# Kernel optimization log

Hardware: AMD Instinct MI355X
Metric: run time of the kernel (lower is better)

Reference implementation:

```python
import jax, jax.numpy as jnp
import numpy as np

EPS = 1e-6
BN_EPS = 1e-5
K = 20

def _vn_linear(x, W):
    # x: [B,C,...] channel axis 1; W: [out,in]
    return jnp.einsum('oc,bc...->bo...', W, x)

def _vn_bn(x):
    # training-mode BatchNorm on per-vector norms (affine at init: gamma=1, beta=0)
    norm = jnp.sqrt(jnp.sum(x * x, axis=2)) + EPS  # [B,C,*spatial]
    axes = (0,) + tuple(range(2, norm.ndim))
    mean = jnp.mean(norm, axis=axes, keepdims=True)
    var = jnp.mean((norm - mean) ** 2, axis=axes, keepdims=True)  # biased, as torch BN
    norm_bn = (norm - mean) / jnp.sqrt(var + BN_EPS)
    return x / jnp.expand_dims(norm, 2) * jnp.expand_dims(norm_bn, 2)

def _vn_llr(x, Wf, Wd, ns=0.0, use_bn=True):
    p = _vn_linear(x, Wf)
    if use_bn:
        p = _vn_bn(p)
    d = _vn_linear(x, Wd)
    dot = jnp.sum(p * d, axis=2, keepdims=True)
    mask = (dot >= 0).astype(x.dtype)
    dsq = jnp.sum(d * d, axis=2, keepdims=True)
    return ns * p + (1.0 - ns) * (mask * p + (1.0 - mask) * (p - dot / (dsq + EPS) * d))

def _graph_feature_cross(x, k):
    # x: [B,3,N] -> [B,3,3,N,k]
    B, _, N = x.shape
    inner = -2.0 * jnp.einsum('bdn,bdm->bnm', x, x)
    xx = jnp.sum(x * x, axis=1)  # [B,N]
    pdist = -xx[:, :, None] - inner - xx[:, None, :]  # [B,N,N]
    idx = jax.lax.top_k(pdist, k)[1]  # [B,N,k] nearest neighbors
    xt = jnp.transpose(x, (0, 2, 1))  # [B,N,3]
    nbr = xt[jnp.arange(B)[:, None, None], idx]  # [B,N,k,3]
    ctr = jnp.broadcast_to(xt[:, :, None, :], nbr.shape)  # [B,N,k,3]
    cross = jnp.cross(nbr, ctr)
    feat = jnp.stack([nbr - ctr, ctr, cross], axis=3)  # [B,N,k,3ch,3vec]
    return jnp.transpose(feat, (0, 3, 4, 1, 2))  # [B,3,3,N,k]

def _forward(points, wposf, wposd, w1f, w1d, w2f, w2d, w3, ws1f, ws1d, ws2f, ws2d, wlin):
    x = jnp.transpose(points, (0, 2, 1))  # [B,3,N]
    B, _, N = x.shape
    feat = _graph_feature_cross(x, K)  # [B,3,3,N,K]
    x = _vn_llr(feat, wposf, wposd)  # conv_pos, dim=5 -> [B,21,3,N,K]
    x = jnp.mean(x, axis=-1)  # mean pool over k -> [B,21,3,N]
    x = _vn_llr(x, w1f, w1d)  # conv1
    x = _vn_llr(x, w2f, w2d)  # conv2 (feature_transform=False so in=21? no: conv2 takes 42 -- matches cat-free path only when feature_transform False? conv2 in=42 but code passes x of 21? original passes 21-ch into conv2 only if feature_transform else 21; here feature_transform=False and conv2 expects 42 in torch -- we mirror with w2f [42,42] applied after duplicating? No: mirror exact torch behavior below.)
    return x

def reference(points, wposf, wposd, w1f, w1d, w2f, w2d, w3, ws1f, ws1d, ws2f, ws2d, wlin):
    x = jnp.transpose(points, (0, 2, 1))  # [B,3,N]
    B, _, N = x.shape
    feat = _graph_feature_cross(x, K)  # [B,3,3,N,K]
    x = _vn_llr(feat, wposf, wposd)  # [B,21,3,N,K]
    x = jnp.mean(x, axis=-1)  # mean pool -> [B,21,3,N]
    x = _vn_llr(x, w1f, w1d)  # [B,21,3,N]
    # torch conv2 is Linear(42,42) but with feature_transform=False it is applied to 21-ch
    # input; nn.Linear would error, so faithful runnable form uses the duplicated-channel
    # convention: concat (x, x) is NOT in the original; instead we slice w2 to [42,21].
    x = _vn_llr(x, w2f[:, :21], w2d[:, :21])  # [B,42,3,N]
    x = _vn_bn(_vn_linear(x, w3))  # conv3 + bn3 -> [B,85,3,N]
    x_mean_out = jnp.mean(x, axis=-1, keepdims=True)  # [B,85,3,1]
    x = jnp.concatenate([x, jnp.broadcast_to(x_mean_out, x.shape)], axis=1)  # [B,170,3,N]
    z = _vn_llr(x, ws1f, ws1d)  # [B,85,3,N]
    z = _vn_llr(z, ws2f, ws2d)  # [B,42,3,N]
    z = _vn_linear(z, wlin)  # [B,3,3,N]
    z = jnp.transpose(z, (0, 2, 1, 3))  # [B,3,3,N]
    x_std = jnp.einsum('bijm,bjkm->bikm', x, z)  # [B,170,3,N]
    xf = x_std.reshape(B, -1, N)  # [B,510,N]
    inv_z = jnp.max(xf, axis=-1)  # [B,510]
    center_loc = jnp.mean(x_mean_out, axis=2)  # [B,85,1]
    return (inv_z, x_mean_out, center_loc)

def setup_inputs() -> dict:
    key = jax.random.key(0)
    ks = jax.random.split(key, 14)
    B, N = 4, 8192
    def w(k, shape):
        return (jax.random.normal(k, shape, dtype=jnp.float32) * (1.0 / np.sqrt(shape[1])))
    return {
        'points': jax.random.normal(ks[0], (B, N, 3), dtype=jnp.float32),
        'wposf': w(ks[1], (21, 3)),
        'wposd': w(ks[2], (21, 3)),
        'w1f': w(ks[3], (21, 21)),
        'w1d': w(ks[4], (21, 21)),
        'w2f': w(ks[5], (42, 42)),
        'w2d': w(ks[6], (42, 42)),
        'w3': w(ks[7], (85, 42)),
        'ws1f': w(ks[8], (85, 170)),
        'ws1d': w(ks[9], (85, 170)),
        'ws2f': w(ks[10], (42, 85)),
        'ws2d': w(ks[11], (42, 85)),
        'wlin': w(ks[12], (3, 42)),
    }
```

## Files before the change

kernel.cpp:

```cpp
#include <hip/hip_runtime.h>
#include <cstdint>
#include <cstddef>

#define EPSF 1e-6f
#define BN_EPSF 1e-5f

constexpr int Bb = 4;
constexpr int Nn = 8192;
constexpr int KK = 20;
constexpr int SEG = 8;
constexpr int SEGLEN = Nn / SEG;
constexpr int BUF = 24;

constexpr size_t KNN0_OFF = 0;
constexpr size_t X1_OFF  = 0;
constexpr size_t X2_OFF  = 2064384;
constexpr size_t X3_OFF  = 4128768;
constexpr size_t Z1_OFF  = 0;
constexpr size_t X4_OFF  = 8355840;
constexpr size_t IDX_OFF = 16711680;
constexpr size_t Z2_OFF  = 17367040;
constexpr size_t Z3_OFF  = 21495808;
constexpr size_t ACC_OFF = 21790720;
constexpr size_t XM_OFF  = 21791744;
constexpr size_t BF_OFF  = 21792764;
constexpr size_t BD_OFF  = 21793784;
constexpr size_t DEXT_OFF = 21795840;
constexpr size_t EXT_NEED = (DEXT_OFF + 8355840) * 4;

__device__ __forceinline__ float wave_sum(float v) {
#pragma unroll
  for (int off = 32; off; off >>= 1) v += __shfl_xor(v, off, 64);
  return v;
}
__device__ __forceinline__ float wave_max(float v) {
#pragma unroll
  for (int off = 32; off; off >>= 1) v = fmaxf(v, __shfl_xor(v, off, 64));
  return v;
}
__device__ __forceinline__ uint32_t umin32(uint32_t a, uint32_t b) { return a < b ? a : b; }
__device__ __forceinline__ uint32_t umax32(uint32_t a, uint32_t b) { return a < b ? b : a; }

__global__ __launch_bounds__(1024) void zero_acc(float* __restrict__ a) {
  a[threadIdx.x] = 0.f;
}

__global__ __launch_bounds__(256) void knn_kernel(const float* __restrict__ pts,
                                                  uint32_t* __restrict__ knnp) {
  __shared__ float4 tile[SEGLEN];
  __shared__ uint32_t buf[BUF * 256];
  const int tid = threadIdx.x;
  const int n = blockIdx.x * 256 + tid;
  const int b = blockIdx.y;
  const int s = blockIdx.z;
  const float* pb = pts + (size_t)b * Nn * 3;

  for (int i = tid; i < SEGLEN; i += 256) {
    const float* p = pb + (size_t)(s * SEGLEN + i) * 3;
    const float x = p[0], y = p[1], z = p[2];
    tile[i] = make_float4(x, y, z, 0.5f * (x * x + y * y + z * z));
  }
  const float qx = pb[n * 3 + 0], qy = pb[n * 3 + 1], qz = pb[n * 3 + 2];
  const float nqx = -qx, nqy = -qy, nqz = -qz;
  const float h = 0.5f * (qx * qx + qy * qy + qz * qz);
  __syncthreads();

  uint32_t keys[KK];
#pragma unroll
  for (int j = 0; j < KK; ++j) keys[j] = 0xFFFFFFFFu;

  const int base = s * SEGLEN;

#pragma unroll 4
  for (int j = 0; j < 64; ++j) {
    const float4 c = tile[j];
    float u = fmaf(nqx, c.x, fmaf(nqy, c.y, fmaf(nqz, c.z, c.w + h)));
    u = fmaxf(u, 0.f);
    uint32_t mx = (__float_as_uint(u) & 0xFFFFE000u) | (uint32_t)(base + j);
#pragma unroll
    for (int q = 0; q < KK; ++q) {
      const uint32_t mn = umin32(keys[q], mx);
      mx = umax32(keys[q], mx);
      keys[q] = mn;
    }
  }

  uint32_t thresh = keys[KK - 1];
  float thresh_up = __uint_as_float((thresh & 0xFFFFE000u) + 0x2000u);
  float th_h = thresh_up - h + 2.4e-7f * fabsf(thresh_up) + 1e-30f;
  int cnt = 0;

  for (int j0 = 64; j0 < SEGLEN; j0 += 4) {
#pragma unroll
    for (int u4 = 0; u4 < 4; ++u4) {
      const int j = j0 + u4;
      const float4 c = tile[j];
      const float up = fmaf(nqx, c.x, fmaf(nqy, c.y, fmaf(nqz, c.z, c.w)));
      if (up < th_h) {
        const float uc = fmaxf(up + h, 0.f);
        buf[cnt * 256 + tid] = (__float_as_uint(uc) & 0xFFFFE000u) | (uint32_t)(base + j);
        ++cnt;
      }
    }
    if (__any(cnt > BUF - 4)) {
#pragma unroll
      for (int i = 0; i < BUF; ++i) {
        uint32_t mx = (i < cnt) ? buf[i * 256 + tid] : 0xFFFFFFFFu;
#pragma unroll
        for (int q = 0; q < KK; ++q) {
          const uint32_t mn = umin32(keys[q], mx);
          mx = umax32(keys[q], mx);
          keys[q] = mn;
        }
      }
      cnt = 0;
      thresh = keys[KK - 1];
      thresh_up = __uint_as_float((thresh & 0xFFFFE000u) + 0x2000u);
      th_h = thresh_up - h + 2.4e-7f * fabsf(thresh_up) + 1e-30f;
    }
  }
#pragma unroll
  for (int i = 0; i < BUF; ++i) {
    uint32_t mx = (i < cnt) ? buf[i * 256 + tid] : 0xFFFFFFFFu;
#pragma unroll
    for (int q = 0; q < KK; ++q) {
      const uint32_t mn = umin32(keys[q], mx);
      mx = umax32(keys[q], mx);
      keys[q] = mn;
    }
  }

  uint32_t* op = knnp + ((size_t)(b * SEG + s) * KK) * Nn + n;
#pragma unroll
  for (int j = 0; j < KK; ++j) op[(size_t)j * Nn] = keys[j];
}

__global__ __launch_bounds__(256) void merge8(const uint32_t* __restrict__ in,
                                              int* __restrict__ idx) {
  const int t = blockIdx.x * 256 + threadIdx.x;
  const int n = t & (Nn - 1), b = t >> 13;
  const uint32_t* base = in + ((size_t)(b * SEG) * KK) * Nn + n;
  uint32_t h[SEG];
  int ii[SEG];
#pragma unroll
  for (int s = 0; s < SEG; ++s) {
    h[s] = base[(size_t)s * KK * Nn];
    ii[s] = 1;
  }
  int* op = idx + (size_t)t * KK;
#pragma unroll
  for (int m = 0; m < KK; ++m) {
    uint32_t k = h[0];
#pragma unroll
    for (int s = 1; s < SEG; ++s) k = umin32(k, h[s]);
    op[m] = (int)(k & 8191u);
#pragma unroll
    for (int s = 0; s < SEG; ++s) {
      if (h[s] == k) {
        h[s] = (ii[s] < KK) ? base[(size_t)s * KK * Nn + (size_t)ii[s] * Nn] : 0xFFFFFFFFu;
        ii[s]++;
      }
    }
  }
}

__global__ __launch_bounds__(256) void s1_stats(const float* __restrict__ pts,
                                                const int* __restrict__ idx,
                                                const float* __restrict__ wf,
                                                float* __restrict__ acc) {
  __shared__ float lacc[42];
  const int tid = threadIdx.x;
  for (int i = tid; i < 42; i += 256) lacc[i] = 0.f;
  __syncthreads();
  const int t = blockIdx.x * 256 + tid;
  const int site = t / 5;
  const int kq = (t % 5) * 4;
  const int n = site & (Nn - 1), b = site >> 13;
  const float* pb = pts + (size_t)b * Nn * 3;
  const float cx = pb[n * 3 + 0], cy = pb[n * 3 + 1], cz = pb[n * 3 + 2];
  float s1a[21], s2a[21];
#pragma unroll
  for (int o = 0; o < 21; ++o) { s1a[o] = 0.f; s2a[o] = 0.f; }
#pragma unroll
  for (int k = kq; k < kq + 4; ++k) {
    const int m = idx[(size_t)site * KK + k];
    const float ax = pb[m * 3 + 0], ay = pb[m * 3 + 1], az = pb[m * 3 + 2];
    const float e0x = ax - cx, e0y = ay - cy, e0z = az - cz;
    const float e2x = ay * cz - az * cy, e2y = az * cx - ax * cz, e2z = ax * cy - ay * cx;
#pragma unroll
    for (int o = 0; o < 21; ++o) {
      const float w0 = wf[o * 3 + 0], w1 = wf[o * 3 + 1], w2 = wf[o * 3 + 2];
      const float px = w0 * e0x + w1 * cx + w2 * e2x;
      const float py = w0 * e0y + w1 * cy + w2 * e2y;
      const float pz = w0 * e0z + w1 * cz + w2 * e2z;
      const float nrm = sqrtf(px * px + py * py + pz * pz) + EPSF;
      s1a[o] += nrm;
      s2a[o] += nrm * nrm;
    }
  }
#pragma unroll
  for (int o = 0; o < 21; ++o) {
    const float s1 = wave_sum(s1a[o]);
    const float s2 = wave_sum(s2a[o]);
    if ((tid & 63) == 0) { atomicAdd(&lacc[o], s1); atomicAdd(&lacc[21 + o], s2); }
  }
  __syncthreads();
  for (int i = tid; i < 42; i += 256) atomicAdd(&acc[i], lacc[i]);
}

__global__ __launch_bounds__(256) void s1_apply(const float* __restrict__ pts,
                                                const int* __restrict__ idx,
                                                const float* __restrict__ wf,
                                                const float* __restrict__ wd,
                                                const float* __restrict__ acc,
                                                float* __restrict__ x1) {
  const int t = blockIdx.x * 256 + threadIdx.x;
  const int o0 = blockIdx.y * 7;
  const int n = t & (Nn - 1), b = t >> 13;
  const float* pb = pts + (size_t)b * Nn * 3;
  const float cx = pb[n * 3 + 0], cy = pb[n * 3 + 1], cz = pb[n * 3 + 2];
  const float inv_cnt = 1.f / (float)(Bb * Nn * KK);
  float meano[7], istdo[7];
#pragma unroll
  for (int j = 0; j < 7; ++j) {
    const float mn = acc[o0 + j] * inv_cnt;
    const float vr = acc[21 + o0 + j] * inv_cnt - mn * mn;
    meano[j] = mn;
    istdo[j] = rsqrtf(vr + BN_EPSF);
  }
  float accu[7][3];
#pragma unroll
  for (int j = 0; j < 7; ++j) { accu[j][0] = 0.f; accu[j][1] = 0.f; accu[j][2] = 0.f; }
  for (int k = 0; k < KK; ++k) {
    const int m = idx[(size_t)t * KK + k];
    const float ax = pb[m * 3 + 0], ay = pb[m * 3 + 1], az = pb[m * 3 + 2];
    const float e0x = ax - cx, e0y = ay - cy, e0z = az - cz;
    const float e2x = ay * cz - az * cy, e2y = az * cx - ax * cz, e2z = ax * cy - ay * cx;
#pragma unroll
    for (int j = 0; j < 7; ++j) {
      const int o = o0 + j;
      const float wf0 = wf[o * 3 + 0], wf1 = wf[o * 3 + 1], wf2 = wf[o * 3 + 2];
      const float px = wf0 * e0x + wf1 * cx + wf2 * e2x;
      const float py = wf0 * e0y + wf1 * cy + wf2 * e2y;
      const float pz = wf0 * e0z + wf1 * cz + wf2 * e2z;
      const float nrm = sqrtf(px * px + py * py + pz * pz) + EPSF;
      const float factor = (nrm - meano[j]) * istdo[j] / nrm;
      const float q0 = px * factor, q1 = py * factor, q2 = pz * factor;
      const float wd0 = wd[o * 3 + 0], wd1 = wd[o * 3 + 1], wd2 = wd[o * 3 + 2];
      const float dx = wd0 * e0x + wd1 * cx + wd2 * e2x;
      const float dy = wd0 * e0y + wd1 * cy + wd2 * e2y;
      const float dz = wd0 * e0z + wd1 * cz + wd2 * e2z;
      const float dot = q0 * dx + q1 * dy + q2 * dz;
      const float dsq = dx * dx + dy * dy + dz * dz;
      const float corr = (dot < 0.f) ? dot / (dsq + EPSF) : 0.f;
      accu[j][0] += q0 - corr * dx;
      accu[j][1] += q1 - corr * dy;
      accu[j][2] += q2 - corr * dz;
    }
  }
  const float sc = 1.f / (float)KK;
  float* ob = x1 + (size_t)b * 21 * 3 * Nn + n;
#pragma unroll
  for (int j = 0; j < 7; ++j) {
    const int o = o0 + j;
    ob[(o * 3 + 0) * Nn] = accu[j][0] * sc;
    ob[(o * 3 + 1) * Nn] = accu[j][1] * sc;
    ob[(o * 3 + 2) * Nn] = accu[j][2] * sc;
  }
}

template <int CIN, int COUT, int OT, bool HAS_BIAS>
__global__ __launch_bounds__(256) void vn_stats_pd(const float* __restrict__ X,
                                                   const float* __restrict__ Wf,
                                                   const float* __restrict__ Wd, int ws,
                                                   const float* __restrict__ biasF,
                                                   const float* __restrict__ biasD,
                                                   float* __restrict__ acc,
                                                   float* __restrict__ P,
                                                   float* __restrict__ D) {
  __shared__ float lacc[2 * OT];
  const int tid = threadIdx.x;
  if (tid < 2 * OT) lacc[tid] = 0.f;
  __syncthreads();
  const int o0 = blockIdx.y * OT;
  const int t = blockIdx.x * 256 + tid;
  const int n = t & (Nn - 1), b = t >> 13;
  const float* xb = X + (size_t)b * CIN * 3 * Nn + n;
  float* pb = P + (size_t)b * COUT * 3 * Nn + n;
  float* db = D + (size_t)b * COUT * 3 * Nn + n;
  float p[OT][3], dv[OT][3];
#pragma unroll
  for (int j = 0; j < OT; ++j)
#pragma unroll
    for (int dd = 0; dd < 3; ++dd) {
      p[j][dd] = HAS_BIAS ? biasF[((size_t)b * COUT + o0 + j) * 3 + dd] : 0.f;
      dv[j][dd] = HAS_BIAS ? biasD[((size_t)b * COUT + o0 + j) * 3 + dd] : 0.f;
    }
  for (int c = 0; c < CIN; ++c) {
    const float x0 = xb[(c * 3 + 0) * Nn];
    const float x1v = xb[(c * 3 + 1) * Nn];
    const float x2v = xb[(c * 3 + 2) * Nn];
#pragma unroll
    for (int j = 0; j < OT; ++j) {
      const float wfv = Wf[(o0 + j) * ws + c];
      p[j][0] += wfv * x0; p[j][1] += wfv * x1v; p[j][2] += wfv * x2v;
      const float wdv = Wd[(o0 + j) * ws + c];
      dv[j][0] += wdv * x0; dv[j][1] += wdv * x1v; dv[j][2] += wdv * x2v;
    }
  }
#pragma unroll
  for (int j = 0; j < OT; ++j) {
    const int o = o0 + j;
    pb[(size_t)(o * 3 + 0) * Nn] = p[j][0];
    pb[(size_t)(o * 3 + 1) * Nn] = p[j][1];
    pb[(size_t)(o * 3 + 2) * Nn] = p[j][2];
    db[(size_t)(o * 3 + 0) * Nn] = dv[j][0];
    db[(size_t)(o * 3 + 1) * Nn] = dv[j][1];
    db[(size_t)(o * 3 + 2) * Nn] = dv[j][2];
  }
#pragma unroll
  for (int j = 0; j < OT; ++j) {
    const float nrm = sqrtf(p[j][0] * p[j][0] + p[j][1] * p[j][1] + p[j][2] * p[j][2]) + EPSF;
    const float s1 = wave_sum(nrm);
    const float s2 = wave_sum(nrm * nrm);
    if ((tid & 63) == 0) { atomicAdd(&lacc[j], s1); atomicAdd(&lacc[OT + j], s2); }
  }
  __syncthreads();
  if (tid < 2 * OT) {
    const int g = (tid < OT) ? (o0 + tid) : (COUT + o0 + (tid - OT));
    atomicAdd(&acc[g], lacc[tid]);
  }
}

template <int CIN, int COUT, int OT, bool HAS_BIAS>
__global__ __launch_bounds__(256) void vn_stats_pd2(const float* __restrict__ X,
                                                    const float* __restrict__ Wf,
                                                    const float* __restrict__ Wd, int ws,
                                                    const float* __restrict__ biasF,
                                                    const float* __restrict__ biasD,
                                                    float* __restrict__ acc,
                                                    float* __restrict__ P,
                                                    float* __restrict__ D) {
  __shared__ float lacc[2 * OT];
  const int tid = threadIdx.x;
  if (tid < 2 * OT) lacc[tid] = 0.f;
  __syncthreads();
  const int o0 = blockIdx.y * OT;
  const int sp = blockIdx.x * 256 + tid;
  const int n = (sp & (Nn / 2 - 1)) * 2, b = sp >> 12;
  const float* xb = X + (size_t)b * CIN * 3 * Nn + n;
  float* pb = P + (size_t)b * COUT * 3 * Nn + n;
  float* db = D + (size_t)b * COUT * 3 * Nn + n;
  float2 p[OT][3], dv[OT][3];
#pragma unroll
  for (int j = 0; j < OT; ++j)
#pragma unroll
    for (int dd = 0; dd < 3; ++dd) {
      const float bf = HAS_BIAS ? biasF[((size_t)b * COUT + o0 + j) * 3 + dd] : 0.f;
      const float bd = HAS_BIAS ? biasD[((size_t)b * COUT + o0 + j) * 3 + dd] : 0.f;
      p[j][dd] = make_float2(bf, bf);
      dv[j][dd] = make_float2(bd, bd);
    }
  for (int c = 0; c < CIN; ++c) {
    const float2 x0 = *(const float2*)(xb + (size_t)(c * 3 + 0) * Nn);
    const float2 x1v = *(const float2*)(xb + (size_t)(c * 3 + 1) * Nn);
    const float2 x2v = *(const float2*)(xb + (size_t)(c * 3 + 2) * Nn);
#pragma unroll
    for (int j = 0; j < OT; ++j) {
      const float wfv = Wf[(o0 + j) * ws + c];
      p[j][0].x += wfv * x0.x;  p[j][0].y += wfv * x0.y;
      p[j][1].x += wfv * x1v.x; p[j][1].y += wfv * x1v.y;
      p[j][2].x += wfv * x2v.x; p[j][2].y += wfv * x2v.y;
      const float wdv = Wd[(o0 + j) * ws + c];
      dv[j][0].x += wdv * x0.x;  dv[j][0].y += wdv * x0.y;
      dv[j][1].x += wdv * x1v.x; dv[j][1].y += wdv * x1v.y;
      dv[j][2].x += wdv * x2v.x; dv[j][2].y += wdv * x2v.y;
    }
  }
#pragma unroll
  for (int j = 0; j < OT; ++j) {
    const int o = o0 + j;
    *(float2*)(pb + (size_t)(o * 3 + 0) * Nn) = p[j][0];
    *(float2*)(pb + (size_t)(o * 3 + 1) * Nn) = p[j][1];
    *(float2*)(pb + (size_t)(o * 3 + 2) * Nn) = p[j][2];
    *(float2*)(db + (size_t)(o * 3 + 0) * Nn) = dv[j][0];
    *(float2*)(db + (size_t)(o * 3 + 1) * Nn) = dv[j][1];
    *(float2*)(db + (size_t)(o * 3 + 2) * Nn) = dv[j][2];
  }
#pragma unroll
  for (int j = 0; j < OT; ++j) {
    const float n0 = sqrtf(p[j][0].x * p[j][0].x + p[j][1].x * p[j][1].x + p[j][2].x * p[j][2].x) + EPSF;
    const float n1 = sqrtf(p[j][0].y * p[j][0].y + p[j][1].y * p[j][1].y + p[j][2].y * p[j][2].y) + EPSF;
    const float s1 = wave_sum(n0 + n1);
    const float s2 = wave_sum(n0 * n0 + n1 * n1);
    if ((tid & 63) == 0) { atomicAdd(&lacc[j], s1); atomicAdd(&lacc[OT + j], s2); }
  }
  __syncthreads();
  if (tid < 2 * OT) {
    const int g = (tid < OT) ? (o0 + tid) : (COUT + o0 + (tid - OT));
    atomicAdd(&acc[g], lacc[tid]);
  }
}

__device__ __forceinline__ float llr_one(float p0, float p1, float p2,
                                         float d0, float d1, float d2,
                                         float mn, float istd,
                                         float& r0o, float& r1o, float& r2o) {
  const float nrm = sqrtf(p0 * p0 + p1 * p1 + p2 * p2) + EPSF;
  const float factor = (nrm - mn) * istd / nrm;
  float r0 = p0 * factor, r1 = p1 * factor, r2 = p2 * factor;
  const float dot = r0 * d0 + r1 * d1 + r2 * d2;
  const float dsq = d0 * d0 + d1 * d1 + d2 * d2;
  const float corr = (dot < 0.f) ? dot / (dsq + EPSF) : 0.f;
  r0o = r0 - corr * d0; r1o = r1 - corr * d1; r2o = r2 - corr * d2;
  return 0.f;
}

template <int COUT>
__global__ __launch_bounds__(256) void vn_llr_ew4(const float* __restrict__ acc, float cntinv,
                                                  float* __restrict__ P,
                                                  const float* __restrict__ D) {
  const int t = blockIdx.x * 256 + threadIdx.x;
  const int n4 = t & (Nn / 4 - 1);
  const int r = t >> 11;
  const int o = r % COUT, b = r / COUT;
  float4* pp = (float4*)(P + ((size_t)(b * COUT + o) * 3) * Nn) + n4;
  const float4* dp = (const float4*)(D + ((size_t)(b * COUT + o) * 3) * Nn) + n4;
  const float4 p0 = pp[0], p1 = pp[Nn / 4], p2 = pp[2 * (Nn / 4)];
  const float4 d0 = dp[0], d1 = dp[Nn / 4], d2 = dp[2 * (Nn / 4)];
  const float mn = acc[o] * cntinv;
  const float vr = acc[COUT + o] * cntinv - mn * mn;
  const float istd = rsqrtf(vr + BN_EPSF);
  float4 r0, r1, r2;
  llr_one(p0.x, p1.x, p2.x, d0.x, d1.x, d2.x, mn, istd, r0.x, r1.x, r2.x);
  llr_one(p0.y, p1.y, p2.y, d0.y, d1.y, d2.y, mn, istd, r0.y, r1.y, r2.y);
  llr_one(p0.z, p1.z, p2.z, d0.z, d1.z, d2.z, mn, istd, r0.z, r1.z, r2.z);
  llr_one(p0.w, p1.w, p2.w, d0.w, d1.w, d2.w, mn, istd, r0.w, r1.w, r2.w);
  pp[0] = r0;
  pp[Nn / 4] = r1;
  pp[2 * (Nn / 4)] = r2;
}

template <int CIN, int COUT, int OT, bool HAS_BIAS>
__global__ __launch_bounds__(256) void vn_stats_pc(const float* __restrict__ X,
                                                   const float* __restrict__ Wf, int ws,
                                                   const float* __restrict__ biasF,
                                                   float* __restrict__ acc,
                                                   float* __restrict__ P) {
  __shared__ float lacc[2 * OT];
  const int tid = threadIdx.x;
  if (tid < 2 * OT) lacc[tid] = 0.f;
  __syncthreads();
  const int o0 = blockIdx.y * OT;
  const int t = blockIdx.x * 256 + tid;
  const int n = t & (Nn - 1), b = t >> 13;
  const float* xb = X + (size_t)b * CIN * 3 * Nn + n;
  float* pb = P + (size_t)b * COUT * 3 * Nn + n;
  float p[OT][3];
#pragma unroll
  for (int j = 0; j < OT; ++j)
#pragma unroll
    for (int dd = 0; dd < 3; ++dd)
      p[j][dd] = HAS_BIAS ? biasF[((size_t)b * COUT + o0 + j) * 3 + dd] : 0.f;
  for (int c = 0; c < CIN; ++c) {
    const float x0 = xb[(c * 3 + 0) * Nn];
    const float x1v = xb[(c * 3 + 1) * Nn];
    const float x2v = xb[(c * 3 + 2) * Nn];
#pragma unroll
    for (int j = 0; j < OT; ++j) {
      const float wv = Wf[(o0 + j) * ws + c];
      p[j][0] += wv * x0; p[j][1] += wv * x1v; p[j][2] += wv * x2v;
    }
  }
#pragma unroll
  for (int j = 0; j < OT; ++j) {
    const int o = o0 + j;
    pb[(size_t)(o * 3 + 0) * Nn] = p[j][0];
    pb[(size_t)(o * 3 + 1) * Nn] = p[j][1];
    pb[(size_t)(o * 3 + 2) * Nn] = p[j][2];
  }
#pragma unroll
  for (int j = 0; j < OT; ++j) {
    const float nrm = sqrtf(p[j][0] * p[j][0] + p[j][1] * p[j][1] + p[j][2] * p[j][2]) + EPSF;
    const float s1 = wave_sum(nrm);
    const float s2 = wave_sum(nrm * nrm);
    if ((tid & 63) == 0) { atomicAdd(&lacc[j], s1); atomicAdd(&lacc[OT + j], s2); }
  }
  __syncthreads();
  if (tid < 2 * OT) {
    const int g = (tid < OT) ? (o0 + tid) : (COUT + o0 + (tid - OT));
    atomicAdd(&acc[g], lacc[tid]);
  }
}

template <int CIN, int COUT, int OT, bool HAS_BIAS>
__global__ __launch_bounds__(256) void vn_stats_pc2(const float* __restrict__ X,
                                                    const float* __restrict__ Wf, int ws,
                                                    const float* __restrict__ biasF,
                                                    float* __restrict__ acc,
                                                    float* __restrict__ P) {
  __shared__ float lacc[2 * OT];
  const int tid = threadIdx.x;
  if (tid < 2 * OT) lacc[tid] = 0.f;
  __syncthreads();
  const int o0 = blockIdx.y * OT;
  const int sp = blockIdx.x * 256 + tid;
  const int n = (sp & (Nn / 2 - 1)) * 2, b = sp >> 12;
  const float* xb = X + (size_t)b * CIN * 3 * Nn + n;
  float* pb = P + (size_t)b * COUT * 3 * Nn + n;
  float2 p[OT][3];
#pragma unroll
  for (int j = 0; j < OT; ++j)
#pragma unroll
    for (int dd = 0; dd < 3; ++dd) {
      const float bf = HAS_BIAS ? biasF[((size_t)b * COUT + o0 + j) * 3 + dd] : 0.f;
      p[j][dd] = make_float2(bf, bf);
    }
  for (int c = 0; c < CIN; ++c) {
    const float2 x0 = *(const float2*)(xb + (size_t)(c * 3 + 0) * Nn);
    const float2 x1v = *(const float2*)(xb + (size_t)(c * 3 + 1) * Nn);
    const float2 x2v = *(const float2*)(xb + (size_t)(c * 3 + 2) * Nn);
#pragma unroll
    for (int j = 0; j < OT; ++j) {
      const float wv = Wf[(o0 + j) * ws + c];
      p[j][0].x += wv * x0.x;  p[j][0].y += wv * x0.y;
      p[j][1].x += wv * x1v.x; p[j][1].y += wv * x1v.y;
      p[j][2].x += wv * x2v.x; p[j][2].y += wv * x2v.y;
    }
  }
#pragma unroll
  for (int j = 0; j < OT; ++j) {
    const int o = o0 + j;
    *(float2*)(pb + (size_t)(o * 3 + 0) * Nn) = p[j][0];
    *(float2*)(pb + (size_t)(o * 3 + 1) * Nn) = p[j][1];
    *(float2*)(pb + (size_t)(o * 3 + 2) * Nn) = p[j][2];
  }
#pragma unroll
  for (int j = 0; j < OT; ++j) {
    const float n0 = sqrtf(p[j][0].x * p[j][0].x + p[j][1].x * p[j][1].x + p[j][2].x * p[j][2].x) + EPSF;
    const float n1 = sqrtf(p[j][0].y * p[j][0].y + p[j][1].y * p[j][1].y + p[j][2].y * p[j][2].y) + EPSF;
    const float s1 = wave_sum(n0 + n1);
    const float s2 = wave_sum(n0 * n0 + n1 * n1);
    if ((tid & 63) == 0) { atomicAdd(&lacc[j], s1); atomicAdd(&lacc[OT + j], s2); }
  }
  __syncthreads();
  if (tid < 2 * OT) {
    const int g = (tid < OT) ? (o0 + tid) : (COUT + o0 + (tid - OT));
    atomicAdd(&acc[g], lacc[tid]);
  }
}

template <int CIN, int COUT, int OT, bool HAS_BIAS>
__global__ __launch_bounds__(256) void vn_apply_pc(const float* __restrict__ X,
                                                   const float* __restrict__ Wd, int ws,
                                                   const float* __restrict__ biasD,
                                                   const float* __restrict__ acc, float cntinv,
                                                   float* __restrict__ P) {
  const int o0 = blockIdx.y * OT;
  const int t = blockIdx.x * 256 + threadIdx.x;
  const int n = t & (Nn - 1), b = t >> 13;
  const float* xb = X + (size_t)b * CIN * 3 * Nn + n;
  float* pb = P + (size_t)b * COUT * 3 * Nn + n;
  float dv[OT][3];
#pragma unroll
  for (int j = 0; j < OT; ++j)
#pragma unroll
    for (int dd = 0; dd < 3; ++dd)
      dv[j][dd] = HAS_BIAS ? biasD[((size_t)b * COUT + o0 + j) * 3 + dd] : 0.f;
  for (int c = 0; c < CIN; ++c) {
    const float x0 = xb[(c * 3 + 0) * Nn];
    const float x1v = xb[(c * 3 + 1) * Nn];
    const float x2v = xb[(c * 3 + 2) * Nn];
#pragma unroll
    for (int j = 0; j < OT; ++j) {
      const float wdv = Wd[(o0 + j) * ws + c];
      dv[j][0] += wdv * x0; dv[j][1] += wdv * x1v; dv[j][2] += wdv * x2v;
    }
  }
#pragma unroll
  for (int j = 0; j < OT; ++j) {
    const int o = o0 + j;
    const float p0 = pb[(size_t)(o * 3 + 0) * Nn];
    const float p1 = pb[(size_t)(o * 3 + 1) * Nn];
    const float p2 = pb[(size_t)(o * 3 + 2) * Nn];
    const float nrm = sqrtf(p0 * p0 + p1 * p1 + p2 * p2) + EPSF;
    const float mn = acc[o] * cntinv;
    const float vr = acc[COUT + o] * cntinv - mn * mn;
    const float factor = (nrm - mn) * rsqrtf(vr + BN_EPSF) / nrm;
    float r0 = p0 * factor, r1 = p1 * factor, r2 = p2 * factor;
    const float dot = r0 * dv[j][0] + r1 * dv[j][1] + r2 * dv[j][2];
    const float dsq = dv[j][0] * dv[j][0] + dv[j][1] * dv[j][1] + dv[j][2] * dv[j][2];
    const float corr = (dot < 0.f) ? dot / (dsq + EPSF) : 0.f;
    r0 -= corr * dv[j][0]; r1 -= corr * dv[j][1]; r2 -= corr * dv[j][2];
    pb[(size_t)(o * 3 + 0) * Nn] = r0;
    pb[(size_t)(o * 3 + 1) * Nn] = r1;
    pb[(size_t)(o * 3 + 2) * Nn] = r2;
  }
}

template <int COUT>
__global__ __launch_bounds__(256) void vn_bn4(const float* __restrict__ acc, float cntinv,
                                              float* __restrict__ P) {
  const int t = blockIdx.x * 256 + threadIdx.x;
  const int n4 = t & (Nn / 4 - 1);
  const int r = t >> 11;
  const int o = r % COUT, b = r / COUT;
  float4* pp = (float4*)(P + ((size_t)(b * COUT + o) * 3) * Nn) + n4;
  const float4 p0 = pp[0], p1 = pp[Nn / 4], p2 = pp[2 * (Nn / 4)];
  const float mn = acc[o] * cntinv;
  const float vr = acc[COUT + o] * cntinv - mn * mn;
  const float istd = rsqrtf(vr + BN_EPSF);
  float4 r0, r1, r2;
#define BN_ONE(f) {                                                        \
    const float nrm = sqrtf(p0.f * p0.f + p1.f * p1.f + p2.f * p2.f) + EPSF; \
    const float factor = (nrm - mn) * istd / nrm;                          \
    r0.f = p0.f * factor; r1.f = p1.f * factor; r2.f = p2.f * factor; }
  BN_ONE(x) BN_ONE(y) BN_ONE(z) BN_ONE(w)
#undef BN_ONE
  pp[0] = r0;
  pp[Nn / 4] = r1;
  pp[2 * (Nn / 4)] = r2;
}

__global__ __launch_bounds__(256) void s5_mean(const float* __restrict__ x4,
                                               float* __restrict__ xm,
                                               float* __restrict__ out) {
  const int row = blockIdx.x;
  const int b = row / 255, rcd = row % 255;
  const float* src = x4 + (size_t)b * 255 * Nn + (size_t)rcd * Nn;
  float s = 0.f;
  for (int n = threadIdx.x; n < Nn; n += 256) s += src[n];
  s = wave_sum(s);
  __shared__ float wsum[4];
  if ((threadIdx.x & 63) == 0) wsum[threadIdx.x >> 6] = s;
  __syncthreads();
  if (threadIdx.x == 0) {
    const float mv = (wsum[0] + wsum[1] + wsum[2] + wsum[3]) * (1.f / (float)Nn);
    xm[row] = mv;
    out[2040 + row] = mv;
  }
}

__global__ __launch_bounds__(256) void s5_bias(const float* __restrict__ xm,
                                               const float* __restrict__ ws1f,
                                               const float* __restrict__ ws1d,
                                               float* __restrict__ biasF,
                                               float* __restrict__ biasD,
                                               float* __restrict__ out) {
  const int t = blockIdx.x * 256 + threadIdx.x;
  if (t < 1020) {
    const int b = t / 255, r = t % 255, o = r / 3, dd = r % 3;
    float sf = 0.f, sd = 0.f;
    for (int c = 0; c < 85; ++c) {
      const float xv = xm[(b * 85 + c) * 3 + dd];
      sf += ws1f[o * 170 + 85 + c] * xv;
      sd += ws1d[o * 170 + 85 + c] * xv;
    }
    biasF[t] = sf;
    biasD[t] = sd;
  }
  if (t < 340) {
    const int b = t / 85, c = t % 85;
    out[3060 + t] = (xm[(b * 85 + c) * 3 + 0] + xm[(b * 85 + c) * 3 + 1] +
                     xm[(b * 85 + c) * 3 + 2]) * (1.f / 3.f);
  }
}

__global__ __launch_bounds__(256) void s8_z3(const float* __restrict__ z2,
                                             const float* __restrict__ wlin,
                                             float* __restrict__ z3) {
  const int t = blockIdx.x * 256 + threadIdx.x;
  const int n = t & (Nn - 1), b = t >> 13;
  const float* zb = z2 + (size_t)b * 42 * 3 * Nn + n;
  float accv[3][3];
#pragma unroll
  for (int o = 0; o < 3; ++o)
#pragma unroll
    for (int dd = 0; dd < 3; ++dd) accv[o][dd] = 0.f;
  for (int c = 0; c < 42; ++c) {
    const float x0 = zb[(c * 3 + 0) * Nn];
    const float x1v = zb[(c * 3 + 1) * Nn];
    const float x2v = zb[(c * 3 + 2) * Nn];
#pragma unroll
    for (int o = 0; o < 3; ++o) {
      const float wv = wlin[o * 42 + c];
      accv[o][0] += wv * x0; accv[o][1] += wv * x1v; accv[o][2] += wv * x2v;
    }
  }
  float* ob = z3 + (size_t)b * 9 * Nn + n;
#pragma unroll
  for (int o = 0; o < 3; ++o)
#pragma unroll
    for (int dd = 0; dd < 3; ++dd) ob[(o * 3 + dd) * Nn] = accv[o][dd];
}

__global__ __launch_bounds__(256) void s9_max(const float* __restrict__ x4,
                                              const float* __restrict__ xm,
                                              const float* __restrict__ z3,
                                              float* __restrict__ out) {
  const int tile = blockIdx.x;
  const int b = blockIdx.y;
  const int i0 = tile * 5;
  const bool upper = (i0 >= 85);
  float mx[15];
#pragma unroll
  for (int r = 0; r < 15; ++r) mx[r] = -3.402823466e38f;
  float xmr[5][3];
  if (upper) {
#pragma unroll
    for (int ii = 0; ii < 5; ++ii)
#pragma unroll
      for (int j = 0; j < 3; ++j) xmr[ii][j] = xm[(b * 85 + (i0 - 85 + ii)) * 3 + j];
  }
  const float* zb = z3 + (size_t)b * 9 * Nn;
  const float* xb = x4 + (size_t)b * 255 * Nn;
  for (int n = threadIdx.x; n < Nn; n += 256) {
    float zk[3][3];
#pragma unroll
    for (int k = 0; k < 3; ++k)
#pragma unroll
      for (int j = 0; j < 3; ++j) zk[k][j] = zb[(k * 3 + j) * Nn + n];
#pragma unroll
    for (int ii = 0; ii < 5; ++ii) {
      float xj0, xj1, xj2;
      if (upper) {
        xj0 = xmr[ii][0]; xj1 = xmr[ii][1]; xj2 = xmr[ii][2];
      } else {
        xj0 = xb[((i0 + ii) * 3 + 0) * Nn + n];
        xj1 = xb[((i0 + ii) * 3 + 1) * Nn + n];
        xj2 = xb[((i0 + ii) * 3 + 2) * Nn + n];
      }
#pragma unroll
      for (int k = 0; k < 3; ++k) {
        const float v = xj0 * zk[k][0] + xj1 * zk[k][1] + xj2 * zk[k][2];
        mx[ii * 3 + k] = fmaxf(mx[ii * 3 + k], v);
      }
    }
  }
  __shared__ float red[4 * 15];
#pragma unroll
  for (int r = 0; r < 15; ++r) {
    const float v = wave_max(mx[r]);
    if ((threadIdx.x & 63) == 0) red[(threadIdx.x >> 6) * 15 + r] = v;
  }
  __syncthreads();
  if (threadIdx.x < 15) {
    const float v = fmaxf(fmaxf(red[threadIdx.x], red[15 + threadIdx.x]),
                          fmaxf(red[30 + threadIdx.x], red[45 + threadIdx.x]));
    out[b * 510 + i0 * 3 + threadIdx.x] = v;
  }
}

extern "C" void kernel_launch(void* const* d_in, const int* in_sizes, int n_in,
                              void* d_out, int out_size, void* d_ws, size_t ws_size,
                              hipStream_t stream) {
  const float* pts   = (const float*)d_in[0];
  const float* wposf = (const float*)d_in[1];
  const float* wposd = (const float*)d_in[2];
  const float* w1f   = (const float*)d_in[3];
  const float* w1d   = (const float*)d_in[4];
  const float* w2f   = (const float*)d_in[5];
  const float* w2d   = (const float*)d_in[6];
  const float* w3    = (const float*)d_in[7];
  const float* ws1f  = (const float*)d_in[8];
  const float* ws1d  = (const float*)d_in[9];
  const float* ws2f  = (const float*)d_in[10];
  const float* ws2d  = (const float*)d_in[11];
  const float* wlin  = (const float*)d_in[12];
  float* out = (float*)d_out;
  float* wsf = (float*)d_ws;

  uint32_t* knnp0 = (uint32_t*)(wsf + KNN0_OFF);
  float* x1 = wsf + X1_OFF;
  float* x2 = wsf + X2_OFF;
  float* x3 = wsf + X3_OFF;
  float* z1 = wsf + Z1_OFF;
  float* x4 = wsf + X4_OFF;
  int* idx  = (int*)(wsf + IDX_OFF);
  float* z2 = wsf + Z2_OFF;
  float* z3 = wsf + Z3_OFF;
  float* acc = wsf + ACC_OFF;
  float* xm = wsf + XM_OFF;
  float* biasF = wsf + BF_OFF;
  float* biasD = wsf + BD_OFF;
  float* d1 = wsf + X3_OFF;
  float* d2 = wsf + X4_OFF;
  float* dext = wsf + DEXT_OFF;
  const bool ext = ws_size >= EXT_NEED;

  const float inv_sites = 1.f / (float)(Bb * Nn);
  const int GP = Bb * Nn / 2 / 256;

  zero_acc<<<1, 1024, 0, stream>>>(acc);
  knn_kernel<<<dim3(Nn / 256, Bb, SEG), 256, 0, stream>>>(pts, knnp0);
  merge8<<<Bb * Nn / 256, 256, 0, stream>>>(knnp0, idx);

  s1_stats<<<Bb * Nn * 5 / 256, 256, 0, stream>>>(pts, idx, wposf, acc + 0);
  s1_apply<<<dim3(Bb * Nn / 256, 3), 256, 0, stream>>>(pts, idx, wposf, wposd, acc + 0, x1);

  vn_stats_pd<21, 21, 7, false><<<dim3(Bb * Nn / 256, 3), 256, 0, stream>>>(
      x1, w1f, w1d, 21, nullptr, nullptr, acc + 64, x2, d1);
  vn_llr_ew4<21><<<Bb * 21 * Nn / 4 / 256, 256, 0, stream>>>(acc + 64, inv_sites, x2, d1);

  vn_stats_pd<21, 42, 7, false><<<dim3(Bb * Nn / 256, 6), 256, 0, stream>>>(
      x2, w2f, w2d, 42, nullptr, nullptr, acc + 128, x3, d2);
  vn_llr_ew4<42><<<Bb * 42 * Nn / 4 / 256, 256, 0, stream>>>(acc + 128, inv_sites, x3, d2);

  vn_stats_pc2<42, 85, 5, false><<<dim3(GP, 17), 256, 0, stream>>>(
      x3, w3, 42, nullptr, acc + 256, x4);
  vn_bn4<85><<<Bb * 85 * Nn / 4 / 256, 256, 0, stream>>>(acc + 256, inv_sites, x4);

  s5_mean<<<Bb * 255, 256, 0, stream>>>(x4, xm, out);
  s5_bias<<<4, 256, 0, stream>>>(xm, ws1f, ws1d, biasF, biasD, out);

  if (ext) {
    vn_stats_pd2<85, 85, 5, true><<<dim3(GP, 17), 256, 0, stream>>>(
        x4, ws1f, ws1d, 170, biasF, biasD, acc + 512, z1, dext);
    vn_llr_ew4<85><<<Bb * 85 * Nn / 4 / 256, 256, 0, stream>>>(acc + 512, inv_sites, z1, dext);
    vn_stats_pd2<85, 42, 7, false><<<dim3(GP, 6), 256, 0, stream>>>(
        z1, ws2f, ws2d, 85, nullptr, nullptr, acc + 768, z2, dext);
    vn_llr_ew4<42><<<Bb * 42 * Nn / 4 / 256, 256, 0, stream>>>(acc + 768, inv_sites, z2, dext);
  } else {
    vn_stats_pc<85, 85, 17, true><<<dim3(Bb * Nn / 256, 5), 256, 0, stream>>>(
        x4, ws1f, 170, biasF, acc + 512, z1);
    vn_apply_pc<85, 85, 17, true><<<dim3(Bb * Nn / 256, 5), 256, 0, stream>>>(
        x4, ws1d, 170, biasD, acc + 512, inv_sites, z1);
    vn_stats_pc<85, 42, 14, false><<<dim3(Bb * Nn / 256, 3), 256, 0, stream>>>(
        z1, ws2f, 85, nullptr, acc + 768, z2);
    vn_apply_pc<85, 42, 14, false><<<dim3(Bb * Nn / 256, 3), 256, 0, stream>>>(
        z1, ws2d, 85, nullptr, acc + 768, inv_sites, z2);
  }

  s8_z3<<<Bb * Nn / 256, 256, 0, stream>>>(z2, wlin, z3);
  s9_max<<<dim3(34, Bb), 256, 0, stream>>>(x4, xm, z3, out);
}
```

Baseline: 647.7 us.

## Fuse BN apply with mean reduction, fold acc zeroing into merge, shorten kNN warmup

Merges the vn_bn4 normalization pass and the s5_mean reduction into one kernel that normalizes x4 in place while accumulating per-channel means, removing one full read of x4. The zeroing of the stats accumulator moves into merge8's first block, dropping a separate launch. The kNN warmup that seeds the top-k list with an exact insertion sort is cut from 64 to 40 candidates. That gives a looser initial threshold, so more candidates may reach the buffered path. The fused kernel uses only 340 blocks, and each walks a full row serially, which may underuse the GPU compared with the old wide elementwise launch.

```diff
diff --git a/kernel.cpp b/kernel.cpp
--- a/kernel.cpp
+++ b/kernel.cpp
@@ -41,10 +41,6 @@
 __device__ __forceinline__ uint32_t umin32(uint32_t a, uint32_t b) { return a < b ? a : b; }
 __device__ __forceinline__ uint32_t umax32(uint32_t a, uint32_t b) { return a < b ? b : a; }
 
-__global__ __launch_bounds__(1024) void zero_acc(float* __restrict__ a) {
-  a[threadIdx.x] = 0.f;
-}
-
 __global__ __launch_bounds__(256) void knn_kernel(const float* __restrict__ pts,
                                                   uint32_t* __restrict__ knnp) {
   __shared__ float4 tile[SEGLEN];
@@ -72,7 +68,7 @@
   const int base = s * SEGLEN;
 
 #pragma unroll 4
-  for (int j = 0; j < 64; ++j) {
+  for (int j = 0; j < 40; ++j) {
     const float4 c = tile[j];
     float u = fmaf(nqx, c.x, fmaf(nqy, c.y, fmaf(nqz, c.z, c.w + h)));
     u = fmaxf(u, 0.f);
@@ -90,7 +86,7 @@
   float th_h = thresh_up - h + 2.4e-7f * fabsf(thresh_up) + 1e-30f;
   int cnt = 0;
 
-  for (int j0 = 64; j0 < SEGLEN; j0 += 4) {
+  for (int j0 = 40; j0 < SEGLEN; j0 += 4) {
 #pragma unroll
     for (int u4 = 0; u4 < 4; ++u4) {
       const int j = j0 + u4;
@@ -136,7 +132,11 @@
 }
 
 __global__ __launch_bounds__(256) void merge8(const uint32_t* __restrict__ in,
-                                              int* __restrict__ idx) {
+                                              int* __restrict__ idx,
+                                              float* __restrict__ accz) {
+  if (blockIdx.x == 0) {
+    for (int i = threadIdx.x; i < 1024; i += 256) accz[i] = 0.f;
+  }
   const int t = blockIdx.x * 256 + threadIdx.x;
   const int n = t & (Nn - 1), b = t >> 13;
   const uint32_t* base = in + ((size_t)(b * SEG) * KK) * Nn + n;
@@ -622,20 +622,33 @@
   pp[2 * (Nn / 4)] = r2;
 }
 
-__global__ __launch_bounds__(256) void s5_mean(const float* __restrict__ x4,
-                                               float* __restrict__ xm,
-                                               float* __restrict__ out) {
-  const int row = blockIdx.x;
-  const int b = row / 255, rcd = row % 255;
-  const float* src = x4 + (size_t)b * 255 * Nn + (size_t)rcd * Nn;
-  float s = 0.f;
-  for (int n = threadIdx.x; n < Nn; n += 256) s += src[n];
-  s = wave_sum(s);
-  __shared__ float wsum[4];
-  if ((threadIdx.x & 63) == 0) wsum[threadIdx.x >> 6] = s;
-  __syncthreads();
-  if (threadIdx.x == 0) {
-    const float mv = (wsum[0] + wsum[1] + wsum[2] + wsum[3]) * (1.f / (float)Nn);
+__global__ __launch_bounds__(256) void s5_bn_mean(const float* __restrict__ acc, float cntinv,
+                                                  float* __restrict__ x4,
+                                                  float* __restrict__ xm,
+                                                  float* __restrict__ out) {
+  const int bc = blockIdx.x;
+  const int b = bc / 85, c = bc % 85;
+  const int tid = threadIdx.x;
+  const float mn = acc[c] * cntinv;
+  const float vr = acc[85 + c] * cntinv - mn * mn;
+  const float istd = rsqrtf(vr + BN_EPSF);
+  float* base = x4 + ((size_t)(b * 85 + c) * 3) * Nn;
+  float s0 = 0.f, s1 = 0.f, s2 = 0.f;
+  for (int n = tid; n < Nn; n += 256) {
+    const float p0 = base[n], p1 = base[Nn + n], p2 = base[2 * Nn + n];
+    const float nrm = sqrtf(p0 * p0 + p1 * p1 + p2 * p2) + EPSF;
+    const float factor = (nrm - mn) * istd / nrm;
+    const float r0 = p0 * factor, r1 = p1 * factor, r2 = p2 * factor;
+    base[n] = r0; base[Nn + n] = r1; base[2 * Nn + n] = r2;
+    s0 += r0; s1 += r1; s2 += r2;
+  }
+  s0 = wave_sum(s0); s1 = wave_sum(s1); s2 = wave_sum(s2);
+  __shared__ float red[4][3];
+  if ((tid & 63) == 0) { red[tid >> 6][0] = s0; red[tid >> 6][1] = s1; red[tid >> 6][2] = s2; }
+  __syncthreads();
+  if (tid < 3) {
+    const float mv = (red[0][tid] + red[1][tid] + red[2][tid] + red[3][tid]) * (1.f / (float)Nn);
+    const int row = bc * 3 + tid;
     xm[row] = mv;
     out[2040 + row] = mv;
   }
@@ -791,9 +804,8 @@
   const float inv_sites = 1.f / (float)(Bb * Nn);
   const int GP = Bb * Nn / 2 / 256;
 
-  zero_acc<<<1, 1024, 0, stream>>>(acc);
   knn_kernel<<<dim3(Nn / 256, Bb, SEG), 256, 0, stream>>>(pts, knnp0);
-  merge8<<<Bb * Nn / 256, 256, 0, stream>>>(knnp0, idx);
+  merge8<<<Bb * Nn / 256, 256, 0, stream>>>(knnp0, idx, acc);
 
   s1_stats<<<Bb * Nn * 5 / 256, 256, 0, stream>>>(pts, idx, wposf, acc + 0);
   s1_apply<<<dim3(Bb * Nn / 256, 3), 256, 0, stream>>>(pts, idx, wposf, wposd, acc + 0, x1);
@@ -808,9 +820,7 @@
 
   vn_stats_pc2<42, 85, 5, false><<<dim3(GP, 17), 256, 0, stream>>>(
       x3, w3, 42, nullptr, acc + 256, x4);
-  vn_bn4<85><<<Bb * 85 * Nn / 4 / 256, 256, 0, stream>>>(acc + 256, inv_sites, x4);
-
-  s5_mean<<<Bb * 255, 256, 0, stream>>>(x4, xm, out);
+  s5_bn_mean<<<Bb * 85, 256, 0, stream>>>(acc + 256, inv_sites, x4, xm, out);
   s5_bias<<<4, 256, 0, stream>>>(xm, ws1f, ws1d, biasF, biasD, out);
 
   if (ext) {
```

Result: no change. 644.2 us (-0.5%).
